# Kernel optimization log

Hardware: AMD Instinct MI355X
Metric: run time of the kernel (lower is better)

## Reference

```python
import jax, jax.numpy as jnp
import numpy as np

B, S, H, NH = 2, 2048, 2048, 16
HD = H // NH

def setup_inputs() -> dict:
    key = jax.random.key(0)
    ks = jax.random.split(key, 6)
    scale = 1.0 / np.sqrt(H)
    return {
        "x": jax.random.normal(ks[0], (B, S, H), dtype=jnp.float32),
        "Wq": jax.random.normal(ks[1], (H, H), dtype=jnp.float32) * scale,
        "Wk": jax.random.normal(ks[2], (H, H), dtype=jnp.float32) * scale,
        "Wv": jax.random.normal(ks[3], (H, H), dtype=jnp.float32) * scale,
        "Wo": jax.random.normal(ks[4], (H, H), dtype=jnp.float32) * scale,
        "bo": jax.random.normal(ks[5], (H,), dtype=jnp.float32) * 0.01,
    }

def reference(x, Wq, Wk, Wv, Wo, bo):
    # nn.Linear convention: y = x @ W.T (W is [out, in])
    q = (x @ Wq.T).reshape(B, S, NH, HD).transpose(0, 2, 1, 3)  # [B,NH,S,HD]
    k = (x @ Wk.T).reshape(B, S, NH, HD).transpose(0, 2, 1, 3)
    v = (x @ Wv.T).reshape(B, S, NH, HD).transpose(0, 2, 1, 3)
    scale = jnp.asarray(HD, x.dtype) ** -0.5
    scores = jnp.einsum('bhqd,bhkd->bhqk', q, k) * scale  # [B,NH,S,S]
    attn = jax.nn.softmax(scores, axis=-1)
    out = jnp.einsum('bhqk,bhkd->bhqd', attn, v)  # [B,NH,S,HD]
    out = out.transpose(0, 2, 1, 3).reshape(B, S, H)
    return out @ Wo.T + bo
```

## Files before the change

kernel.cpp:

```cpp
#include <hip/hip_runtime.h>
#include <hip/hip_bf16.h>
#include <stdint.h>

#define S_LEN 2048
#define NHEADS 16
#define HDIM 128
#define H_TOT 2048
#define BATCH 2
#define M_TOK 4096
#define KDIM 2048

typedef __attribute__((ext_vector_type(8))) short bf16x8;
typedef __attribute__((ext_vector_type(4))) float f32x4;
typedef __attribute__((ext_vector_type(16))) float f32x16;

__device__ inline ushort bf16rn(float f) {
  union { float f; uint32_t u; } x; x.f = f;
  uint32_t r = x.u + 0x7FFF + ((x.u >> 16) & 1);
  return (ushort)(r >> 16);
}

__global__ __launch_bounds__(256) void cvt_bf16_kernel(const float* __restrict__ in,
                                                       ushort* __restrict__ out, int n4) {
  int i = blockIdx.x * blockDim.x + threadIdx.x;
  int stride = gridDim.x * blockDim.x;
  for (; i < n4; i += stride) {
    float4 v = reinterpret_cast<const float4*>(in)[i];
    ushort4 o;
    o.x = bf16rn(v.x); o.y = bf16rn(v.y); o.z = bf16rn(v.z); o.w = bf16rn(v.w);
    reinterpret_cast<ushort4*>(out)[i] = o;
  }
}

__global__ __launch_bounds__(256) void cvt4_bf16_kernel(const float* __restrict__ w0,
                                                        const float* __restrict__ w1,
                                                        const float* __restrict__ w2,
                                                        const float* __restrict__ w3,
                                                        ushort* __restrict__ o0,
                                                        ushort* __restrict__ o1,
                                                        ushort* __restrict__ o2,
                                                        ushort* __restrict__ o3) {
  const int N4 = KDIM * KDIM / 4;
  int i = blockIdx.x * blockDim.x + threadIdx.x;
  int stride = gridDim.x * blockDim.x;
  for (; i < 4 * N4; i += stride) {
    int seg = i >> 20, off = i & (N4 - 1);
    const float* in = (seg == 0) ? w0 : (seg == 1) ? w1 : (seg == 2) ? w2 : w3;
    ushort* out = (seg == 0) ? o0 : (seg == 1) ? o1 : (seg == 2) ? o2 : o3;
    float4 v = reinterpret_cast<const float4*>(in)[off];
    ushort4 o;
    o.x = bf16rn(v.x); o.y = bf16rn(v.y); o.z = bf16rn(v.z); o.w = bf16rn(v.w);
    reinterpret_cast<ushort4*>(out)[off] = o;
  }
}

template<int MODE>
__global__ __launch_bounds__(256) void gemm_nt(const ushort* __restrict__ A,
                                               const ushort* __restrict__ Bw,
                                               void* __restrict__ Cout,
                                               const float* __restrict__ bias,
                                               float scale) {
  __shared__ ushort As[128 * 32];
  __shared__ ushort Bs[128 * 32];
  const int K = KDIM;
  int tid = threadIdx.x;
  int wave = tid >> 6, lane = tid & 63;
  int bid = blockIdx.x;
  int c = bid & 7, ii = bid >> 3;
  int bx = (c & 1) * 8 + (ii & 7);
  int by = (c >> 1) * 8 + (ii >> 3);
  int bm = by * 128, bn = bx * 128;
  int wr = wave >> 1, wc = wave & 1;

  f32x4 acc[4][4];
#pragma unroll
  for (int i = 0; i < 4; i++)
#pragma unroll
    for (int j = 0; j < 4; j++) acc[i][j] = (f32x4){0.f, 0.f, 0.f, 0.f};

  int r0 = wave * 32 + (lane >> 2);
  int c8 = (lane & 3) * 8;
  const ushort* gA0 = A + (size_t)(bm + r0) * K + c8;
  const ushort* gA1 = gA0 + 16 * (size_t)K;
  const ushort* gB0 = Bw + (size_t)(bn + r0) * K + c8;
  const ushort* gB1 = gB0 + 16 * (size_t)K;
  ushort* lA0 = As + (wave * 2 + 0) * 512;
  ushort* lA1 = As + (wave * 2 + 1) * 512;
  ushort* lB0 = Bs + (wave * 2 + 0) * 512;
  ushort* lB1 = Bs + (wave * 2 + 1) * 512;

  int aoff = (wr * 64 + (lane & 15)) * 32 + (lane >> 4) * 8;
  int boff = (wc * 64 + (lane & 15)) * 32 + (lane >> 4) * 8;

  for (int kt = 0; kt < K; kt += 32) {
    __builtin_amdgcn_global_load_lds((const __attribute__((address_space(1))) void*)gA0,
                                     (__attribute__((address_space(3))) void*)lA0, 16, 0, 0);
    __builtin_amdgcn_global_load_lds((const __attribute__((address_space(1))) void*)gA1,
                                     (__attribute__((address_space(3))) void*)lA1, 16, 0, 0);
    __builtin_amdgcn_global_load_lds((const __attribute__((address_space(1))) void*)gB0,
                                     (__attribute__((address_space(3))) void*)lB0, 16, 0, 0);
    __builtin_amdgcn_global_load_lds((const __attribute__((address_space(1))) void*)gB1,
                                     (__attribute__((address_space(3))) void*)lB1, 16, 0, 0);
    __syncthreads();

    bf16x8 af[4], bfm[4];
#pragma unroll
    for (int i = 0; i < 4; i++) af[i] = *reinterpret_cast<const bf16x8*>(&As[aoff + i * 512]);
#pragma unroll
    for (int j = 0; j < 4; j++) bfm[j] = *reinterpret_cast<const bf16x8*>(&Bs[boff + j * 512]);
#pragma unroll
    for (int i = 0; i < 4; i++)
#pragma unroll
      for (int j = 0; j < 4; j++)
        acc[i][j] = __builtin_amdgcn_mfma_f32_16x16x32_bf16(af[i], bfm[j], acc[i][j], 0, 0, 0);
    __syncthreads();

    gA0 += 32; gA1 += 32; gB0 += 32; gB1 += 32;
  }

  int rbase = bm + wr * 64 + (lane >> 4) * 4;
  int cbase = bn + wc * 64 + (lane & 15);
  if (MODE == 2) {
    float* Cf = (float*)Cout;
#pragma unroll
    for (int j = 0; j < 4; j++) {
      int n = cbase + j * 16;
      float bv = bias[n];
#pragma unroll
      for (int i = 0; i < 4; i++)
#pragma unroll
        for (int q = 0; q < 4; q++) {
          int m = rbase + i * 16 + q;
          Cf[(size_t)m * H_TOT + n] = acc[i][j][q] + bv;
        }
    }
  } else {
    ushort* Cb = (ushort*)Cout;
#pragma unroll
    for (int j = 0; j < 4; j++) {
      int n = cbase + j * 16;
      int h = n >> 7, d = n & 127;
#pragma unroll
      for (int i = 0; i < 4; i++)
#pragma unroll
        for (int q = 0; q < 4; q++) {
          int m = rbase + i * 16 + q;
          int b = m >> 11, s = m & 2047;
          int bh = b * NHEADS + h;
          size_t idx;
          if (MODE == 0) {
            idx = (((size_t)(bh * 64 + (s >> 5)) * 8 + (d >> 4)) * 64 +
                   ((d >> 3) & 1) * 32 + (s & 31)) * 8 + (d & 7);
          } else {
            int r = s & 15;
            int e = (r & 3) | ((r >> 1) & 4);
            int hi = (r >> 2) & 1;
            idx = (((size_t)(bh * 64 + (s >> 5)) * 8 + ((s >> 4) & 1) * 4 + (d >> 5)) * 64 +
                   hi * 32 + (d & 31)) * 8 + e;
          }
          Cb[idx] = bf16rn(acc[i][j][q] * scale);
        }
    }
  }
}

__global__ __launch_bounds__(128) void attn_kernel(const ushort* __restrict__ Qf,
                                                   const ushort* __restrict__ Kf,
                                                   const ushort* __restrict__ Vf,
                                                   ushort* __restrict__ Ob) {
  __shared__ __attribute__((aligned(16))) ushort KV[2][8192];
  __shared__ float lsinv[2][32];
  int lane = threadIdx.x & 63, wave = threadIdx.x >> 6;
  int hi = lane >> 5;

  int bid = blockIdx.x;
  int swz = (bid & 7) * 128 + (bid >> 3);
  int bh = swz >> 5, qt = swz & 31;
  int b = bh >> 4, h = bh & 15;
  int qrow0 = qt * 64 + wave * 32;

  const bf16x8* Qv = reinterpret_cast<const bf16x8*>(Qf) +
                     ((size_t)(bh * 64 + qt * 2 + wave) * 8) * 64 + lane;
  bf16x8 qf[8];
#pragma unroll
  for (int kc = 0; kc < 8; kc++) qf[kc] = Qv[kc * 64];

  f32x16 oacc[4];
#pragma unroll
  for (int d32 = 0; d32 < 4; d32++)
#pragma unroll
    for (int r = 0; r < 16; r++) oacc[d32][r] = 0.f;
  float lsum = 0.f;
  int laneoff = lane * 8;
  const ushort* sbase = wave ? Vf : Kf;

#define STAGE(kt, bufsel)                                                                   \
  {                                                                                         \
    size_t gc = ((size_t)(bh * 64 + (kt))) * 8;                                             \
    _Pragma("unroll") for (int i_ = 0; i_ < 8; i_++) {                                      \
      __builtin_amdgcn_global_load_lds(                                                     \
          (const __attribute__((address_space(1))) void*)(sbase + (gc + i_) * 512 + laneoff),\
          (__attribute__((address_space(3))) void*)(&KV[bufsel][(wave * 8 + i_) * 512]),    \
          16, 0, 0);                                                                        \
    }                                                                                       \
  }

  union pu { bf16x8 v; uint32_t u[4]; };
  pu paA0, paA1, paB0, paB1;
  bf16x8 vrA[8], vrB[8];
  const bf16x8 bz = {0, 0, 0, 0, 0, 0, 0, 0};
#pragma unroll
  for (int j = 0; j < 4; j++) { paA0.u[j] = 0; paA1.u[j] = 0; }
#pragma unroll
  for (int i = 0; i < 8; i++) vrA[i] = bz;

  STAGE(0, 0);
  asm volatile("s_waitcnt vmcnt(0)" ::: "memory");
  __syncthreads();

  const int NT = S_LEN / 32;

#define BODY(T, PI0, PI1, VI, PO0, PO1, VO)                                                 \
  {                                                                                         \
    if ((T) + 1 < NT) STAGE((T) + 1, ((T) + 1) & 1);                                        \
    const ushort* lb = &KV[(T) & 1][0];                                                     \
    f32x16 S;                                                                               \
    _Pragma("unroll") for (int r = 0; r < 16; r++) S[r] = 0.f;                              \
    __builtin_amdgcn_s_setprio(1);                                                          \
    _Pragma("unroll") for (int kc = 0; kc < 8; kc++) {                                      \
      bf16x8 kfr = *reinterpret_cast<const bf16x8*>(&lb[kc * 512 + laneoff]);               \
      S = __builtin_amdgcn_mfma_f32_32x32x16_bf16(kfr, qf[kc], S, 0, 0, 0);                 \
    }                                                                                       \
    _Pragma("unroll") for (int d32 = 0; d32 < 4; d32++) {                                   \
      oacc[d32] = __builtin_amdgcn_mfma_f32_32x32x16_bf16(PI0.v, VI[d32], oacc[d32], 0, 0, 0); \
      oacc[d32] = __builtin_amdgcn_mfma_f32_32x32x16_bf16(PI1.v, VI[4 + d32], oacc[d32], 0, 0, 0); \
    }                                                                                       \
    __builtin_amdgcn_s_setprio(0);                                                          \
    float p_[16];                                                                           \
    _Pragma("unroll") for (int r = 0; r < 16; r++) { p_[r] = exp2f(S[r]); lsum += p_[r]; }  \
    _Pragma("unroll") for (int j = 0; j < 4; j++) {                                         \
      uint32_t w0_, w1_;                                                                    \
      asm("v_cvt_pk_bf16_f32 %0, %1, %2" : "=v"(w0_) : "v"(p_[2 * j]), "v"(p_[2 * j + 1])); \
      asm("v_cvt_pk_bf16_f32 %0, %1, %2" : "=v"(w1_) : "v"(p_[8 + 2 * j]), "v"(p_[9 + 2 * j])); \
      PO0.u[j] = w0_; PO1.u[j] = w1_;                                                       \
    }                                                                                       \
    _Pragma("unroll") for (int i_ = 0; i_ < 8; i_++)                                        \
      VO[i_] = *reinterpret_cast<const bf16x8*>(&lb[4096 + i_ * 512 + laneoff]);            \
    asm volatile("s_waitcnt vmcnt(0)" ::: "memory");                                        \
    __syncthreads();                                                                        \
  }

  for (int t = 0; t < NT; t += 2) {
    BODY(t,     paA0, paA1, vrA, paB0, paB1, vrB);
    BODY(t + 1, paB0, paB1, vrB, paA0, paA1, vrA);
  }
#pragma unroll
  for (int d32 = 0; d32 < 4; d32++) {
    oacc[d32] = __builtin_amdgcn_mfma_f32_32x32x16_bf16(paA0.v, vrA[d32], oacc[d32], 0, 0, 0);
    oacc[d32] = __builtin_amdgcn_mfma_f32_32x32x16_bf16(paA1.v, vrA[4 + d32], oacc[d32], 0, 0, 0);
  }

  float total = lsum + __shfl_xor(lsum, 32);
  if (lane < 32) lsinv[wave][lane] = 1.0f / total;
  __syncthreads();

  float ls[16];
#pragma unroll
  for (int r = 0; r < 16; r++) ls[r] = lsinv[wave][(r & 3) + 8 * (r >> 2) + 4 * hi];
#pragma unroll
  for (int d32 = 0; d32 < 4; d32++)
#pragma unroll
    for (int r = 0; r < 16; r++) {
      int row = (r & 3) + 8 * (r >> 2) + 4 * hi;
      size_t idx = ((size_t)(b * S_LEN + qrow0 + row)) * H_TOT + h * HDIM + d32 * 32 + (lane & 31);
      Ob[idx] = bf16rn(oacc[d32][r] * ls[r]);
    }
#undef BODY
#undef STAGE
}

extern "C" void kernel_launch(void* const* d_in, const int* in_sizes, int n_in,
                              void* d_out, int out_size, void* d_ws, size_t ws_size,
                              hipStream_t stream) {
  const float* x  = (const float*)d_in[0];
  const float* Wq = (const float*)d_in[1];
  const float* Wk = (const float*)d_in[2];
  const float* Wv = (const float*)d_in[3];
  const float* Wo = (const float*)d_in[4];
  const float* bo = (const float*)d_in[5];
  float* out = (float*)d_out;

  char* w = (char*)d_ws;
  ushort* xb  = (ushort*)w; w += (size_t)M_TOK * KDIM * 2;
  ushort* Wqb = (ushort*)w; w += (size_t)KDIM * KDIM * 2;
  ushort* Wkb = (ushort*)w; w += (size_t)KDIM * KDIM * 2;
  ushort* Wvb = (ushort*)w; w += (size_t)KDIM * KDIM * 2;
  ushort* Wob = (ushort*)w; w += (size_t)KDIM * KDIM * 2;
  ushort* Qh  = (ushort*)w; w += (size_t)M_TOK * KDIM * 2;
  ushort* Kh  = (ushort*)w; w += (size_t)M_TOK * KDIM * 2;
  ushort* Vt  = (ushort*)w; w += (size_t)M_TOK * KDIM * 2;
  ushort* Ob  = (ushort*)w; w += (size_t)M_TOK * KDIM * 2;

  hipLaunchKernelGGL(cvt_bf16_kernel, dim3(2048), dim3(256), 0, stream, x, xb, M_TOK * KDIM / 4);
  hipLaunchKernelGGL(cvt4_bf16_kernel, dim3(2048), dim3(256), 0, stream,
                     Wq, Wk, Wv, Wo, Wqb, Wkb, Wvb, Wob);

  const float sl = 0.08838834764831845f * 1.4426950408889634f;
  dim3 g(512), blk(256);
  hipLaunchKernelGGL((gemm_nt<0>), g, blk, 0, stream, xb, Wqb, (void*)Qh, (const float*)nullptr, sl);
  hipLaunchKernelGGL((gemm_nt<0>), g, blk, 0, stream, xb, Wkb, (void*)Kh, (const float*)nullptr, 1.0f);
  hipLaunchKernelGGL((gemm_nt<1>), g, blk, 0, stream, xb, Wvb, (void*)Vt, (const float*)nullptr, 1.0f);

  hipLaunchKernelGGL(attn_kernel, dim3(1024), dim3(128), 0, stream, Qh, Kh, Vt, Ob);

  hipLaunchKernelGGL((gemm_nt<2>), g, blk, 0, stream, Ob, Wob, (void*)out, bo, 1.0f);
}
```

Baseline: 301.7 us.

## Replace GEMMs with pre-tiled 256-row double-buffered kernel and fuse QKV projection

Conversion kernels now write x and the weights in a pre-tiled bf16 panel layout, so the GEMM can stream contiguous panels into LDS. A new 512-thread GEMM uses 256-row tiles, 64-wide K steps and double-buffered LDS with interleaved load and MFMA phases and priority hints. Q, K and V are computed in one launch over a concatenated weight, and the attention kernel writes its output straight into the pre-tiled layout the output projection expects. The goal is to cut global and LDS traffic, launch count and load stalls, at the cost of larger LDS use and heavier register pressure.

```diff
diff --git a/kernel.cpp b/kernel.cpp
--- a/kernel.cpp
+++ b/kernel.cpp
@@ -20,135 +20,179 @@
   return (ushort)(r >> 16);
 }
 
-__global__ __launch_bounds__(256) void cvt_bf16_kernel(const float* __restrict__ in,
-                                                       ushort* __restrict__ out, int n4) {
-  int i = blockIdx.x * blockDim.x + threadIdx.x;
-  int stride = gridDim.x * blockDim.x;
-  for (; i < n4; i += stride) {
-    float4 v = reinterpret_cast<const float4*>(in)[i];
-    ushort4 o;
-    o.x = bf16rn(v.x); o.y = bf16rn(v.y); o.z = bf16rn(v.z); o.w = bf16rn(v.w);
-    reinterpret_cast<ushort4*>(out)[i] = o;
-  }
-}
-
-__global__ __launch_bounds__(256) void cvt4_bf16_kernel(const float* __restrict__ w0,
-                                                        const float* __restrict__ w1,
-                                                        const float* __restrict__ w2,
-                                                        const float* __restrict__ w3,
-                                                        ushort* __restrict__ o0,
-                                                        ushort* __restrict__ o1,
-                                                        ushort* __restrict__ o2,
-                                                        ushort* __restrict__ o3) {
-  const int N4 = KDIM * KDIM / 4;
-  int i = blockIdx.x * blockDim.x + threadIdx.x;
-  int stride = gridDim.x * blockDim.x;
-  for (; i < 4 * N4; i += stride) {
-    int seg = i >> 20, off = i & (N4 - 1);
-    const float* in = (seg == 0) ? w0 : (seg == 1) ? w1 : (seg == 2) ? w2 : w3;
-    ushort* out = (seg == 0) ? o0 : (seg == 1) ? o1 : (seg == 2) ? o2 : o3;
-    float4 v = reinterpret_cast<const float4*>(in)[off];
-    ushort4 o;
-    o.x = bf16rn(v.x); o.y = bf16rn(v.y); o.z = bf16rn(v.z); o.w = bf16rn(v.w);
-    reinterpret_cast<ushort4*>(out)[off] = o;
-  }
-}
-
-template<int MODE>
-__global__ __launch_bounds__(256) void gemm_nt(const ushort* __restrict__ A,
-                                               const ushort* __restrict__ Bw,
-                                               void* __restrict__ Cout,
-                                               const float* __restrict__ bias,
-                                               float scale) {
-  __shared__ ushort As[128 * 32];
-  __shared__ ushort Bs[128 * 32];
-  const int K = KDIM;
+template<int ROWS, int PERM>
+__global__ __launch_bounds__(256) void prep_kernel(const float* __restrict__ p0,
+                                                   const float* __restrict__ p1,
+                                                   const float* __restrict__ p2,
+                                                   ushort* __restrict__ out) {
+  __shared__ __attribute__((aligned(16))) ushort tile[ROWS * 64];
+  int kt = blockIdx.x, bt = blockIdx.y, tid = threadIdx.x;
+  int mt = (bt * ROWS) >> 11;
+  const float* src = (mt == 0) ? p0 : (mt == 1) ? p1 : p2;
+  int rowbase = bt * ROWS - (mt << 11);
+  const int IT = ROWS / 32;
+#pragma unroll
+  for (int i = 0; i < IT; i++) {
+    int g = i * 256 + tid, row = g >> 3, k8 = g & 7;
+    const float4* s4 = reinterpret_cast<const float4*>(
+        src + (size_t)(rowbase + row) * KDIM + kt * 64 + k8 * 8);
+    float4 a = s4[0], b = s4[1];
+    union { ushort u[8]; bf16x8 v; } w;
+    w.u[0] = bf16rn(a.x); w.u[1] = bf16rn(a.y); w.u[2] = bf16rn(a.z); w.u[3] = bf16rn(a.w);
+    w.u[4] = bf16rn(b.x); w.u[5] = bf16rn(b.y); w.u[6] = bf16rn(b.z); w.u[7] = bf16rn(b.w);
+    int fr = row >> 4;
+    int p = (PERM == 0) ? (((fr >> 2) & 1) * 8 + ((fr >> 3) & 1) * 4 + (fr & 3))
+          : (PERM == 1) ? (((fr >> 1) & 1) * 8 + (fr >> 2) * 2 + (fr & 1))
+                        : ((fr & 1) * 4 + (fr >> 1));
+    *reinterpret_cast<bf16x8*>(
+        &tile[(p * 2 + (k8 >> 2)) * 512 + ((k8 & 3) * 16 + (row & 15)) * 8]) = w.v;
+  }
+  __syncthreads();
+  ushort* op = out + ((size_t)bt * 32 + kt) * (ROWS * 64);
+#pragma unroll
+  for (int i = 0; i < IT; i++) {
+    int g = i * 256 + tid;
+    reinterpret_cast<bf16x8*>(op)[g] = reinterpret_cast<const bf16x8*>(tile)[g];
+  }
+}
+
+template<int MODE, int FNW, int CHX>
+__global__ __launch_bounds__(512, 2) void gemm8(const ushort* __restrict__ Apre,
+                                                const ushort* __restrict__ Bpre,
+                                                void* __restrict__ C0,
+                                                void* __restrict__ C1,
+                                                void* __restrict__ C2,
+                                                const float* __restrict__ bias,
+                                                float scale) {
+  const int BN = FNW * 64;
+  const int NLB = FNW / 2;
+  const int CHBH = BN / 16;
+  const int BUFB = 32768 + BN * 128;
+  const int NKT = KDIM / 64;
+  const int PANELA = 16384;
+  const int PANELB = BN * 64;
+  __shared__ __attribute__((aligned(16))) char lds[2 * (32768 + FNW * 64 * 128)];
+
   int tid = threadIdx.x;
   int wave = tid >> 6, lane = tid & 63;
+  int lanelo = lane & 15, lanehi = lane >> 4;
+  int wr = wave >> 2, wc = wave & 3;
+
   int bid = blockIdx.x;
-  int c = bid & 7, ii = bid >> 3;
-  int bx = (c & 1) * 8 + (ii & 7);
-  int by = (c >> 1) * 8 + (ii >> 3);
-  int bm = by * 128, bn = bx * 128;
-  int wr = wave >> 1, wc = wave & 1;
-
-  f32x4 acc[4][4];
-#pragma unroll
-  for (int i = 0; i < 4; i++)
-#pragma unroll
-    for (int j = 0; j < 4; j++) acc[i][j] = (f32x4){0.f, 0.f, 0.f, 0.f};
-
-  int r0 = wave * 32 + (lane >> 2);
-  int c8 = (lane & 3) * 8;
-  const ushort* gA0 = A + (size_t)(bm + r0) * K + c8;
-  const ushort* gA1 = gA0 + 16 * (size_t)K;
-  const ushort* gB0 = Bw + (size_t)(bn + r0) * K + c8;
-  const ushort* gB1 = gB0 + 16 * (size_t)K;
-  ushort* lA0 = As + (wave * 2 + 0) * 512;
-  ushort* lA1 = As + (wave * 2 + 1) * 512;
-  ushort* lB0 = Bs + (wave * 2 + 0) * 512;
-  ushort* lB1 = Bs + (wave * 2 + 1) * 512;
-
-  int aoff = (wr * 64 + (lane & 15)) * 32 + (lane >> 4) * 8;
-  int boff = (wc * 64 + (lane & 15)) * 32 + (lane >> 4) * 8;
-
-  for (int kt = 0; kt < K; kt += 32) {
-    __builtin_amdgcn_global_load_lds((const __attribute__((address_space(1))) void*)gA0,
-                                     (__attribute__((address_space(3))) void*)lA0, 16, 0, 0);
-    __builtin_amdgcn_global_load_lds((const __attribute__((address_space(1))) void*)gA1,
-                                     (__attribute__((address_space(3))) void*)lA1, 16, 0, 0);
-    __builtin_amdgcn_global_load_lds((const __attribute__((address_space(1))) void*)gB0,
-                                     (__attribute__((address_space(3))) void*)lB0, 16, 0, 0);
-    __builtin_amdgcn_global_load_lds((const __attribute__((address_space(1))) void*)gB1,
-                                     (__attribute__((address_space(3))) void*)lB1, 16, 0, 0);
-    __syncthreads();
-
-    bf16x8 af[4], bfm[4];
-#pragma unroll
-    for (int i = 0; i < 4; i++) af[i] = *reinterpret_cast<const bf16x8*>(&As[aoff + i * 512]);
-#pragma unroll
-    for (int j = 0; j < 4; j++) bfm[j] = *reinterpret_cast<const bf16x8*>(&Bs[boff + j * 512]);
-#pragma unroll
-    for (int i = 0; i < 4; i++)
-#pragma unroll
-      for (int j = 0; j < 4; j++)
-        acc[i][j] = __builtin_amdgcn_mfma_f32_16x16x32_bf16(af[i], bfm[j], acc[i][j], 0, 0, 0);
-    __syncthreads();
-
-    gA0 += 32; gA1 += 32; gB0 += 32; gB1 += 32;
-  }
-
-  int rbase = bm + wr * 64 + (lane >> 4) * 4;
-  int cbase = bn + wc * 64 + (lane & 15);
+  int xcd = bid & 7, ii = bid >> 3;
+  int bx = xcd * CHX + ii % CHX, by = ii / CHX;
+  int bm = by * 256, bn = bx * BN;
+
+  const ushort* pa0 = Apre + (size_t)by * NKT * PANELA;
+  const ushort* pb0 = Bpre + (size_t)bx * NKT * PANELB;
+
+#define GLD(SRC, DST)                                                                     \
+  __builtin_amdgcn_global_load_lds((const __attribute__((address_space(1))) void*)(SRC),  \
+                                   (__attribute__((address_space(3))) void*)(DST), 16, 0, 0)
+#define STAGE_B(PB, SB)                                                                   \
+  { _Pragma("unroll") for (int h_ = 0; h_ < 2; h_++)                                      \
+      _Pragma("unroll") for (int j_ = 0; j_ < NLB; j_++) {                                \
+        int ch_ = h_ * CHBH + j_ * 8 + wave;                                              \
+        GLD((PB) + ch_ * 512 + lane * 8, (SB) + 32768 + ch_ * 1024 + lane * 16); } }
+#define STAGE_A(PA, SB, H)                                                                \
+  { _Pragma("unroll") for (int j_ = 0; j_ < 2; j_++) {                                    \
+        int ch_ = (H) * 16 + j_ * 8 + wave;                                               \
+        GLD((PA) + ch_ * 512 + lane * 8, (SB) + ch_ * 1024 + lane * 16); } }
+#define READ_A(RB, MH)                                                                    \
+  { _Pragma("unroll") for (int fm_ = 0; fm_ < 4; fm_++)                                   \
+      _Pragma("unroll") for (int kh_ = 0; kh_ < 2; kh_++)                                 \
+        afr[fm_][kh_] = *reinterpret_cast<const bf16x8*>(                                 \
+            (RB) + ((((MH) * 8 + wr * 4 + fm_) * 2 + kh_) * 1024) + lane * 16); }
+#define READ_B(RB, NH)                                                                    \
+  { _Pragma("unroll") for (int fn_ = 0; fn_ < FNW / 2; fn_++)                             \
+      _Pragma("unroll") for (int kh_ = 0; kh_ < 2; kh_++)                                 \
+        bfr[(NH) * (FNW / 2) + fn_][kh_] = *reinterpret_cast<const bf16x8*>(              \
+            (RB) + 32768 +                                                                \
+            ((((NH) * (2 * FNW) + wc * (FNW / 2) + fn_) * 2 + kh_) * 1024) + lane * 16); }
+#define MFPH(MH, NH)                                                                      \
+  { __builtin_amdgcn_s_setprio(1);                                                        \
+    _Pragma("unroll") for (int fm_ = 0; fm_ < 4; fm_++)                                   \
+      _Pragma("unroll") for (int fn_ = 0; fn_ < FNW / 2; fn_++)                           \
+        _Pragma("unroll") for (int kh_ = 0; kh_ < 2; kh_++)                               \
+          acc[(MH) * 4 + fm_][(NH) * (FNW / 2) + fn_] =                                   \
+              __builtin_amdgcn_mfma_f32_16x16x32_bf16(                                    \
+                  afr[fm_][kh_], bfr[(NH) * (FNW / 2) + fn_][kh_],                        \
+                  acc[(MH) * 4 + fm_][(NH) * (FNW / 2) + fn_], 0, 0, 0);                  \
+    __builtin_amdgcn_s_setprio(0); }
+#define BARR __builtin_amdgcn_s_barrier()
+#define SCB __builtin_amdgcn_sched_barrier(0)
+
+  f32x4 acc[8][FNW];
+#pragma unroll
+  for (int i = 0; i < 8; i++)
+#pragma unroll
+    for (int j = 0; j < FNW; j++) acc[i][j] = (f32x4){0.f, 0.f, 0.f, 0.f};
+  bf16x8 afr[4][2], bfr[FNW][2];
+
+  STAGE_B(pb0, lds);
+  STAGE_A(pa0, lds, 0);
+  STAGE_A(pa0, lds, 1);
+  asm volatile("s_waitcnt vmcnt(2)" ::: "memory");
+  SCB; BARR; SCB;
+
+  for (int t = 0; t < NKT; t++) {
+    const char* rb = lds + (t & 1) * BUFB;
+    char* sb = lds + ((t + 1) & 1) * BUFB;
+    const ushort* pa1 = pa0 + (size_t)(t + 1) * PANELA;
+    const ushort* pb1 = pb0 + (size_t)(t + 1) * PANELB;
+    bool stg = (t + 1 < NKT);
+    READ_A(rb, 0); READ_B(rb, 0);
+    if (stg) STAGE_B(pb1, sb);
+    BARR; MFPH(0, 0); BARR; SCB;
+    READ_B(rb, 1);
+    if (stg) STAGE_A(pa1, sb, 0);
+    BARR; MFPH(0, 1);
+    if (stg) {
+      if constexpr (FNW == 4) asm volatile("s_waitcnt vmcnt(6)" ::: "memory");
+      else                    asm volatile("s_waitcnt vmcnt(4)" ::: "memory");
+    } else {
+      asm volatile("s_waitcnt vmcnt(0)" ::: "memory");
+    }
+    SCB; BARR; SCB;
+    READ_A(rb, 1);
+    if (stg) STAGE_A(pa1, sb, 1);
+    BARR; MFPH(1, 1); BARR; SCB;
+    MFPH(1, 0);
+    if (stg) asm volatile("s_waitcnt vmcnt(2)" ::: "memory");
+    SCB; BARR; SCB;
+  }
+
   if (MODE == 2) {
-    float* Cf = (float*)Cout;
-#pragma unroll
-    for (int j = 0; j < 4; j++) {
-      int n = cbase + j * 16;
+    float* Cf = (float*)C0;
+#pragma unroll
+    for (int bi = 0; bi < FNW; bi++) {
+      int n = bn + wc * (FNW * 16) + bi * 16 + lanelo;
       float bv = bias[n];
 #pragma unroll
-      for (int i = 0; i < 4; i++)
+      for (int ai = 0; ai < 8; ai++)
 #pragma unroll
         for (int q = 0; q < 4; q++) {
-          int m = rbase + i * 16 + q;
-          Cf[(size_t)m * H_TOT + n] = acc[i][j][q] + bv;
+          int m = bm + wr * 128 + ai * 16 + lanehi * 4 + q;
+          Cf[(size_t)m * H_TOT + n] = acc[ai][bi][q] + bv;
         }
     }
   } else {
-    ushort* Cb = (ushort*)Cout;
-#pragma unroll
-    for (int j = 0; j < 4; j++) {
-      int n = cbase + j * 16;
+    int seg = bn >> 11;
+    ushort* dst = (seg == 0) ? (ushort*)C0 : (seg == 1) ? (ushort*)C1 : (ushort*)C2;
+    float sc = (seg == 0) ? scale : 1.0f;
+#pragma unroll
+    for (int bi = 0; bi < FNW; bi++) {
+      int n = (bn & 2047) + wc * (FNW * 16) + bi * 16 + lanelo;
       int h = n >> 7, d = n & 127;
 #pragma unroll
-      for (int i = 0; i < 4; i++)
+      for (int ai = 0; ai < 8; ai++)
 #pragma unroll
         for (int q = 0; q < 4; q++) {
-          int m = rbase + i * 16 + q;
+          int m = bm + wr * 128 + ai * 16 + lanehi * 4 + q;
           int b = m >> 11, s = m & 2047;
           int bh = b * NHEADS + h;
           size_t idx;
-          if (MODE == 0) {
+          if (seg < 2) {
             idx = (((size_t)(bh * 64 + (s >> 5)) * 8 + (d >> 4)) * 64 +
                    ((d >> 3) & 1) * 32 + (s & 31)) * 8 + (d & 7);
           } else {
@@ -158,16 +202,24 @@
             idx = (((size_t)(bh * 64 + (s >> 5)) * 8 + ((s >> 4) & 1) * 4 + (d >> 5)) * 64 +
                    hi * 32 + (d & 31)) * 8 + e;
           }
-          Cb[idx] = bf16rn(acc[i][j][q] * scale);
+          dst[idx] = bf16rn(acc[ai][bi][q] * sc);
         }
     }
   }
+#undef GLD
+#undef STAGE_B
+#undef STAGE_A
+#undef READ_A
+#undef READ_B
+#undef MFPH
+#undef BARR
+#undef SCB
 }
 
 __global__ __launch_bounds__(128) void attn_kernel(const ushort* __restrict__ Qf,
                                                    const ushort* __restrict__ Kf,
                                                    const ushort* __restrict__ Vf,
-                                                   ushort* __restrict__ Ob) {
+                                                   ushort* __restrict__ Obpre) {
   __shared__ __attribute__((aligned(16))) ushort KV[2][8192];
   __shared__ float lsinv[2][32];
   int lane = threadIdx.x & 63, wave = threadIdx.x >> 6;
@@ -177,7 +229,6 @@
   int swz = (bid & 7) * 128 + (bid >> 3);
   int bh = swz >> 5, qt = swz & 31;
   int b = bh >> 4, h = bh & 15;
-  int qrow0 = qt * 64 + wave * 32;
 
   const bf16x8* Qv = reinterpret_cast<const bf16x8*>(Qf) +
                      ((size_t)(bh * 64 + qt * 2 + wave) * 8) * 64 + lane;
@@ -264,17 +315,30 @@
   if (lane < 32) lsinv[wave][lane] = 1.0f / total;
   __syncthreads();
 
-  float ls[16];
-#pragma unroll
-  for (int r = 0; r < 16; r++) ls[r] = lsinv[wave][(r & 3) + 8 * (r >> 2) + 4 * hi];
+  ushort* ot = (ushort*)&KV[0][0];
 #pragma unroll
   for (int d32 = 0; d32 < 4; d32++)
 #pragma unroll
     for (int r = 0; r < 16; r++) {
       int row = (r & 3) + 8 * (r >> 2) + 4 * hi;
-      size_t idx = ((size_t)(b * S_LEN + qrow0 + row)) * H_TOT + h * HDIM + d32 * 32 + (lane & 31);
-      Ob[idx] = bf16rn(oacc[d32][r] * ls[r]);
+      float ls = lsinv[wave][row];
+      ot[(wave * 32 + row) * 128 + d32 * 32 + (lane & 31)] = bf16rn(oacc[d32][r] * ls);
     }
+  __syncthreads();
+  int m0 = b * 2048 + qt * 64;
+  int tid = threadIdx.x;
+#pragma unroll
+  for (int i = 0; i < 8; i++) {
+    int g = i * 128 + tid;
+    int rl = g >> 4, k8g = g & 15;
+    int m = m0 + rl;
+    int kcol = h * 128 + k8g * 8;
+    int fm = (m & 255) >> 4;
+    int pA = ((fm >> 2) & 1) * 8 + ((fm >> 3) & 1) * 4 + (fm & 3);
+    size_t off = (((size_t)(m >> 8) * 32 + (kcol >> 6)) * 32 + pA * 2 + ((k8g >> 2) & 1)) * 512 +
+                 (size_t)((k8g & 3) * 16 + (m & 15)) * 8;
+    *reinterpret_cast<bf16x8*>(Obpre + off) = *reinterpret_cast<const bf16x8*>(ot + g * 8);
+  }
 #undef BODY
 #undef STAGE
 }
@@ -291,27 +355,26 @@
   float* out = (float*)d_out;
 
   char* w = (char*)d_ws;
-  ushort* xb  = (ushort*)w; w += (size_t)M_TOK * KDIM * 2;
-  ushort* Wqb = (ushort*)w; w += (size_t)KDIM * KDIM * 2;
-  ushort* Wkb = (ushort*)w; w += (size_t)KDIM * KDIM * 2;
-  ushort* Wvb = (ushort*)w; w += (size_t)KDIM * KDIM * 2;
-  ushort* Wob = (ushort*)w; w += (size_t)KDIM * KDIM * 2;
-  ushort* Qh  = (ushort*)w; w += (size_t)M_TOK * KDIM * 2;
-  ushort* Kh  = (ushort*)w; w += (size_t)M_TOK * KDIM * 2;
-  ushort* Vt  = (ushort*)w; w += (size_t)M_TOK * KDIM * 2;
-  ushort* Ob  = (ushort*)w; w += (size_t)M_TOK * KDIM * 2;
-
-  hipLaunchKernelGGL(cvt_bf16_kernel, dim3(2048), dim3(256), 0, stream, x, xb, M_TOK * KDIM / 4);
-  hipLaunchKernelGGL(cvt4_bf16_kernel, dim3(2048), dim3(256), 0, stream,
-                     Wq, Wk, Wv, Wo, Wqb, Wkb, Wvb, Wob);
+  ushort* Apre  = (ushort*)w; w += (size_t)M_TOK * KDIM * 2;
+  ushort* Bpre  = (ushort*)w; w += (size_t)3 * KDIM * KDIM * 2;
+  ushort* WoPre = (ushort*)w; w += (size_t)KDIM * KDIM * 2;
+  ushort* Qh    = (ushort*)w; w += (size_t)M_TOK * KDIM * 2;
+  ushort* Kh    = (ushort*)w; w += (size_t)M_TOK * KDIM * 2;
+  ushort* Vt    = (ushort*)w; w += (size_t)M_TOK * KDIM * 2;
+  ushort* Obpre = (ushort*)w; w += (size_t)M_TOK * KDIM * 2;
+
+  hipLaunchKernelGGL((prep_kernel<256, 0>), dim3(32, 16), dim3(256), 0, stream,
+                     x, x + (size_t)2048 * KDIM, x, Apre);
+  hipLaunchKernelGGL((prep_kernel<256, 1>), dim3(32, 24), dim3(256), 0, stream, Wq, Wk, Wv, Bpre);
+  hipLaunchKernelGGL((prep_kernel<128, 2>), dim3(32, 16), dim3(256), 0, stream, Wo, Wo, Wo, WoPre);
 
   const float sl = 0.08838834764831845f * 1.4426950408889634f;
-  dim3 g(512), blk(256);
-  hipLaunchKernelGGL((gemm_nt<0>), g, blk, 0, stream, xb, Wqb, (void*)Qh, (const float*)nullptr, sl);
-  hipLaunchKernelGGL((gemm_nt<0>), g, blk, 0, stream, xb, Wkb, (void*)Kh, (const float*)nullptr, 1.0f);
-  hipLaunchKernelGGL((gemm_nt<1>), g, blk, 0, stream, xb, Wvb, (void*)Vt, (const float*)nullptr, 1.0f);
-
-  hipLaunchKernelGGL(attn_kernel, dim3(1024), dim3(128), 0, stream, Qh, Kh, Vt, Ob);
-
-  hipLaunchKernelGGL((gemm_nt<2>), g, blk, 0, stream, Ob, Wob, (void*)out, bo, 1.0f);
-}
+
+  hipLaunchKernelGGL((gemm8<0, 4, 3>), dim3(384), dim3(512), 0, stream,
+                     Apre, Bpre, (void*)Qh, (void*)Kh, (void*)Vt, (const float*)nullptr, sl);
+
+  hipLaunchKernelGGL(attn_kernel, dim3(1024), dim3(128), 0, stream, Qh, Kh, Vt, Obpre);
+
+  hipLaunchKernelGGL((gemm8<2, 2, 2>), dim3(256), dim3(512), 0, stream,
+                     Obpre, WoPre, (void*)out, nullptr, nullptr, bo, 1.0f);
+}
```

New measurement: 283.7 us. 5.9% less time.
